# Kernel tuning notes

Hardware: AMD Instinct MI355X
Metric: run time of the kernel (lower is better)

Reference implementation:

```python
import jax, jax.numpy as jnp
import numpy as np

D_MODEL = 192
D_STATE = 16
D_CONV = 3
EXPAND = 2
D_INNER = EXPAND * D_MODEL  # 384
DT_RANK = (D_MODEL + 15) // 16  # 12 ('auto' = ceil(d_model/16))
B, H, W = 4, 48, 48


def setup_inputs() -> dict:
    key = jax.random.key(0)
    ks = jax.random.split(key, 8)
    s = 0.02
    n = lambda k, sh: (jax.random.normal(k, sh) * s).astype(jnp.float32)
    # 4 Mamba param sets stacked: [w_fwd, w_rev, h_fwd, h_rev]
    return {
        "x": jax.random.normal(ks[0], (B, H, W, D_MODEL), jnp.float32),
        "in_proj_w": n(ks[1], (4, 2 * D_INNER, D_MODEL)),
        "conv_w": n(ks[2], (4, D_INNER, D_CONV)),
        "conv_b": n(ks[3], (4, D_INNER)),
        "x_proj_w": n(ks[4], (4, DT_RANK + 2 * D_STATE, D_INNER)),
        "dt_proj_w": (jax.random.normal(ks[5], (4, D_INNER, DT_RANK)) * (DT_RANK ** -0.5)).astype(jnp.float32),
        "dt_proj_b": (-4.6 + 0.5 * jax.random.normal(ks[6], (4, D_INNER))).astype(jnp.float32),
        "A_log": jnp.broadcast_to(jnp.log(jnp.arange(1, D_STATE + 1, dtype=jnp.float32)), (4, D_INNER, D_STATE)) + jnp.zeros((4, D_INNER, D_STATE), jnp.float32),
        "D": jnp.ones((4, D_INNER), jnp.float32),
        "out_proj_w": n(ks[7], (4, D_MODEL, D_INNER)),
        "norm_w": jnp.ones((D_MODEL,), jnp.float32),
        "norm_b": jnp.zeros((D_MODEL,), jnp.float32),
    }


def _causal_conv(x, w, b):
    # x: [B,L,Di], w: [Di,K] depthwise, causal (pad left K-1, truncate to L)
    K = w.shape[1]
    L = x.shape[1]
    xp = jnp.pad(x, ((0, 0), (K - 1, 0), (0, 0)))
    y = b
    for k in range(K):
        y = y + xp[:, k:k + L, :] * w[:, k]
    return y


def _mamba(u, inW, cW, cB, xpW, dtW, dtB, Alog, Dp, outW):
    # u: [B,L,C]
    R = dtW.shape[1]
    N = Alog.shape[1]
    xz = u @ inW.T                         # [B,L,2*Di]
    xh, z = jnp.split(xz, 2, axis=-1)
    xc = jax.nn.silu(_causal_conv(xh, cW, cB))  # [B,L,Di]
    xdbl = xc @ xpW.T                      # [B,L,R+2N]
    dt = xdbl[..., :R]
    Bm = xdbl[..., R:R + N]
    Cm = xdbl[..., R + N:]
    delta = jax.nn.softplus(dt @ dtW.T + dtB)   # [B,L,Di]
    A = -jnp.exp(Alog)                     # [Di,N]

    def step(h, t):
        d_t, u_t, b_t, c_t = t             # [B,Di],[B,Di],[B,N],[B,N]
        h = jnp.exp(d_t[..., None] * A) * h + (d_t * u_t)[..., None] * b_t[:, None, :]
        return h, jnp.sum(h * c_t[:, None, :], axis=-1)

    h0 = jnp.zeros((u.shape[0], Alog.shape[0], N), u.dtype)
    _, ys = jax.lax.scan(step, h0, (jnp.swapaxes(delta, 0, 1), jnp.swapaxes(xc, 0, 1), jnp.swapaxes(Bm, 0, 1), jnp.swapaxes(Cm, 0, 1)))
    y = jnp.swapaxes(ys, 0, 1) + xc * Dp   # [B,L,Di]
    return (y * jax.nn.silu(z)) @ outW.T   # [B,L,C]


def _bimamba(u, i, P):
    p = lambda j: tuple(t[j] for t in P)
    # NOTE: per the original code, reversed-branch output is NOT flipped back
    return _mamba(u, *p(i)) + _mamba(u[:, ::-1], *p(i + 1))


def _ln(x, w, b):
    m = x.mean(-1, keepdims=True)
    v = ((x - m) ** 2).mean(-1, keepdims=True)
    return (x - m) / jnp.sqrt(v + 1e-5) * w + b


def reference(x, in_proj_w, conv_w, conv_b, x_proj_w, dt_proj_w, dt_proj_b, A_log, D, out_proj_w, norm_w, norm_b):
    Bb, Hh, Ww, C = x.shape
    P = (in_proj_w, conv_w, conv_b, x_proj_w, dt_proj_w, dt_proj_b, A_log, D, out_proj_w)
    # 'b h w c -> b (w h) c'
    xw = jnp.swapaxes(x, 1, 2).reshape(Bb, Ww * Hh, C)
    xw = _bimamba(xw, 0, P)
    # 'b (w h) c -> b (h w) c'
    xh = jnp.swapaxes(xw.reshape(Bb, Ww, Hh, C), 1, 2).reshape(Bb, Hh * Ww, C)
    xh = _ln(xh, norm_w, norm_b) + x.reshape(Bb, -1, C)
    xh = _bimamba(xh, 2, P)
    return xh.reshape(Bb, Hh, Ww, C)
```

## Files before the change

kernel.cpp:

```cpp
#include <hip/hip_runtime.h>
#include <math.h>

#define NB 4
#define NH 48
#define NW 48
#define NC 192
#define NL 2304
#define NM 9216
#define DIN 384
#define XD 44
#define DTR 12
#define CH 24
#define NCHUNK 96

typedef __attribute__((ext_vector_type(8))) short bf16x8;
typedef __attribute__((ext_vector_type(4))) float f32x4;

__device__ inline short f2bf(float f) {
  unsigned u = __builtin_bit_cast(unsigned, f);
  unsigned r = (u + 0x7fffu + ((u >> 16) & 1u)) >> 16;
  return (short)r;
}
__device__ inline float bf2f(short s) {
  unsigned u = ((unsigned)(unsigned short)s) << 16;
  return __builtin_bit_cast(float, u);
}
__device__ inline float fexp2(float x) { return __builtin_amdgcn_exp2f(x); }
__device__ inline float flog2(float x) { return __builtin_amdgcn_logf(x); }
#define LOG2E 1.4426950408889634f
#define LN2   0.6931471805599453f

#define GBM 128
#define GBN 64
#define GBK 32
__global__ __launch_bounds__(256) void mgemm(
    const float* __restrict__ A, int lda,
    const float* __restrict__ Wt,
    float* __restrict__ Cm, int ldc,
    int N, int K, int zA, int zW, int zC)
{
  A  += (size_t)blockIdx.z * zA;
  Wt += (size_t)blockIdx.z * zW;
  Cm += (size_t)blockIdx.z * zC;
  __shared__ short AsH[4][GBM+2][8], AsL[4][GBM+2][8];
  __shared__ short BsH[4][GBN+2][8], BsL[4][GBN+2][8];
  const int tid = threadIdx.x;
  const int l = tid & 63;
  const int wv = tid >> 6;
  const int wr = wv >> 1, wc = wv & 1;
  const int bm = blockIdx.y * GBM;
  const int bn = blockIdx.x * GBN;
  const int lrow = l & 15;
  const int lkb = l >> 4;

  f32x4 acc[4][2];
  #pragma unroll
  for (int mi = 0; mi < 4; ++mi)
    #pragma unroll
    for (int ni = 0; ni < 2; ++ni) acc[mi][ni] = (f32x4)0.f;

  for (int k0 = 0; k0 < K; k0 += GBK) {
    #pragma unroll
    for (int i = 0; i < 2; ++i) {
      int o = tid + i*256;
      int row = o >> 2, kb = o & 3;
      const float* src = A + (size_t)(bm + row)*lda + k0 + kb*8;
      float4 v0 = *(const float4*)src;
      float4 v1 = *(const float4*)(src + 4);
      float vv[8] = {v0.x,v0.y,v0.z,v0.w,v1.x,v1.y,v1.z,v1.w};
      bf16x8 hi, lo;
      #pragma unroll
      for (int j = 0; j < 8; ++j) {
        short h = f2bf(vv[j]);
        hi[j] = h;
        lo[j] = f2bf(vv[j] - bf2f(h));
      }
      *(bf16x8*)&AsH[kb][row][0] = hi;
      *(bf16x8*)&AsL[kb][row][0] = lo;
    }
    {
      int n = tid >> 2, kb = tid & 3;
      float4 v0 = make_float4(0.f,0.f,0.f,0.f), v1 = v0;
      if (bn + n < N) {
        const float* src = Wt + (size_t)(bn + n)*K + k0 + kb*8;
        v0 = *(const float4*)src;
        v1 = *(const float4*)(src + 4);
      }
      float vv[8] = {v0.x,v0.y,v0.z,v0.w,v1.x,v1.y,v1.z,v1.w};
      bf16x8 hi, lo;
      #pragma unroll
      for (int j = 0; j < 8; ++j) {
        short h = f2bf(vv[j]);
        hi[j] = h;
        lo[j] = f2bf(vv[j] - bf2f(h));
      }
      *(bf16x8*)&BsH[kb][n][0] = hi;
      *(bf16x8*)&BsL[kb][n][0] = lo;
    }
    __syncthreads();
    bf16x8 ah[4], al[4], bh[2], bl[2];
    #pragma unroll
    for (int mi = 0; mi < 4; ++mi) {
      int row = wr*64 + mi*16 + lrow;
      ah[mi] = *(const bf16x8*)&AsH[lkb][row][0];
      al[mi] = *(const bf16x8*)&AsL[lkb][row][0];
    }
    #pragma unroll
    for (int ni = 0; ni < 2; ++ni) {
      int rn = wc*32 + ni*16 + lrow;
      bh[ni] = *(const bf16x8*)&BsH[lkb][rn][0];
      bl[ni] = *(const bf16x8*)&BsL[lkb][rn][0];
    }
    #pragma unroll
    for (int mi = 0; mi < 4; ++mi)
      #pragma unroll
      for (int ni = 0; ni < 2; ++ni) {
        acc[mi][ni] = __builtin_amdgcn_mfma_f32_16x16x32_bf16(ah[mi], bh[ni], acc[mi][ni], 0, 0, 0);
        acc[mi][ni] = __builtin_amdgcn_mfma_f32_16x16x32_bf16(ah[mi], bl[ni], acc[mi][ni], 0, 0, 0);
        acc[mi][ni] = __builtin_amdgcn_mfma_f32_16x16x32_bf16(al[mi], bh[ni], acc[mi][ni], 0, 0, 0);
      }
    __syncthreads();
  }
  #pragma unroll
  for (int mi = 0; mi < 4; ++mi)
    #pragma unroll
    for (int ni = 0; ni < 2; ++ni) {
      int n = bn + wc*32 + ni*16 + lrow;
      if (n < N) {
        #pragma unroll
        for (int r = 0; r < 4; ++r) {
          int m = bm + wr*64 + mi*16 + lkb*4 + r;
          Cm[(size_t)m*ldc + n] = acc[mi][ni][r];
        }
      }
    }
}

__global__ __launch_bounds__(256) void transpose_in(const float* __restrict__ x, float* __restrict__ u1)
{
  int idx = blockIdx.x*256 + threadIdx.x;
  int c = idx % NC;
  int rr = idx / NC;
  int s1 = rr % NL;
  int b  = rr / NL;
  int hh = s1 % NH;
  int ww = s1 / NH;
  u1[idx] = x[(((size_t)b*NH + hh)*NW + ww)*NC + c];
}

__global__ __launch_bounds__(256) void conv_silu(
    const float* __restrict__ xz, const float* __restrict__ cw, const float* __restrict__ cb,
    float* __restrict__ xc, int pi)
{
  int idx = blockIdx.x*256 + threadIdx.x;
  int d2 = idx % 768;
  int r  = idx / 768;
  int s  = r % NL;
  int dir = d2 / 384;
  int d = d2 - dir*384;
  int p = pi + dir;
  const float* w = cw + ((size_t)p*DIN + d)*3;
  float acc = cb[p*DIN + d];
  const float* col = xz + (size_t)(r - s)*1536 + (dir*768 + d);
  if (dir == 0) {
    if (s >= 2) acc = fmaf(w[0], col[(size_t)(s-2)*1536], acc);
    if (s >= 1) acc = fmaf(w[1], col[(size_t)(s-1)*1536], acc);
    acc = fmaf(w[2], col[(size_t)s*1536], acc);
  } else {
    if (s+2 < NL) acc = fmaf(w[0], col[(size_t)(s+2)*1536], acc);
    if (s+1 < NL) acc = fmaf(w[1], col[(size_t)(s+1)*1536], acc);
    acc = fmaf(w[2], col[(size_t)s*1536], acc);
  }
  float sg = 1.f / (1.f + fexp2(-acc*LOG2E));
  xc[idx] = acc * sg;
}

__global__ __launch_bounds__(384) void scan_pass1(
    const float* __restrict__ xc, const float* __restrict__ xdbl,
    const float* __restrict__ dtw, const float* __restrict__ dtb,
    const float* __restrict__ alog, float* __restrict__ ws2,
    float* __restrict__ dlt_out, int pi)
{
  const int chunk = blockIdx.x;
  const int bd = blockIdx.y;
  const int b = bd >> 1, dir = bd & 1;
  const int d = threadIdx.x;
  const int p = pi + dir;
  __shared__ float sX[CH][28];
  for (int e = d; e < CH*28; e += 384) {
    int t = e / 28, q = e - t*28;
    int sseq = chunk*CH + t;
    int s = dir ? (NL-1-sseq) : sseq;
    sX[t][q] = xdbl[((size_t)b*NL + s)*88 + dir*XD + q];
  }
  float wdt[DTR];
  #pragma unroll
  for (int k = 0; k < DTR; ++k) wdt[k] = dtw[((size_t)p*DIN + d)*DTR + k];
  const float bdt = dtb[(size_t)p*DIN + d];
  float Ar2[16], h[16];
  #pragma unroll
  for (int n = 0; n < 16; ++n) {
    Ar2[n] = -__expf(alog[((size_t)p*DIN + d)*16 + n]) * LOG2E;
    h[n] = 0.f;
  }
  float cum = 0.f;
  __syncthreads();
  #pragma unroll 2
  for (int t = 0; t < CH; ++t) {
    int sseq = chunk*CH + t;
    int s = dir ? (NL-1-sseq) : sseq;
    size_t row = (size_t)b*NL + s;
    float u = xc[row*768 + dir*384 + d];
    float acc = bdt;
    #pragma unroll
    for (int k = 0; k < DTR; ++k) acc = fmaf(sX[t][k], wdt[k], acc);
    float e1 = fexp2(-fabsf(acc)*LOG2E);
    float dlt = fmaxf(acc, 0.f) + LN2*flog2(1.f + e1);
    cum += dlt;
    dlt_out[row*768 + dir*384 + d] = dlt;
    float du = dlt * u;
    #pragma unroll
    for (int n = 0; n < 16; ++n) {
      float a = fexp2(dlt * Ar2[n]);
      h[n] = fmaf(a, h[n], du * sX[t][12+n]);
    }
  }
  size_t base = ((size_t)bd*NCHUNK + chunk)*32*384 + d;
  #pragma unroll
  for (int n = 0; n < 16; ++n) {
    ws2[base + (size_t)n*384] = fexp2(cum * Ar2[n]);
    ws2[base + (size_t)(16+n)*384] = h[n];
  }
}

__global__ __launch_bounds__(256) void scan_prefix(float* __restrict__ ws2)
{
  int g = blockIdx.x*256 + threadIdx.x;
  int d = g % 384;
  int rest = g / 384;
  int n = rest & 15;
  int bd = rest >> 4;
  float hin = 0.f;
  size_t base = ((size_t)bd*NCHUNK*32 + n)*384 + d;
  for (int j = 0; j < NCHUNK; j += 8) {
    float Pv[8], hv[8];
    #pragma unroll
    for (int u = 0; u < 8; ++u) {
      size_t ip = base + (size_t)(j+u)*32*384;
      Pv[u] = ws2[ip];
      hv[u] = ws2[ip + (size_t)16*384];
    }
    #pragma unroll
    for (int u = 0; u < 8; ++u) {
      size_t ip = base + (size_t)(j+u)*32*384;
      ws2[ip + (size_t)16*384] = hin;
      hin = fmaf(Pv[u], hin, hv[u]);
    }
  }
}

__global__ __launch_bounds__(384) void scan_pass2(
    const float* __restrict__ xc, const float* __restrict__ xz,
    const float* __restrict__ xdbl, const float* __restrict__ alog,
    const float* __restrict__ dvec, const float* __restrict__ ws2,
    float* __restrict__ gio, int pi)
{
  const int chunk = blockIdx.x;
  const int bd = blockIdx.y;
  const int b = bd >> 1, dir = bd & 1;
  const int d = threadIdx.x;
  const int p = pi + dir;
  __shared__ float sX[CH][32];
  for (int e = d; e < CH*32; e += 384) {
    int t = e / 32, q = e - t*32;
    int sseq = chunk*CH + t;
    int s = dir ? (NL-1-sseq) : sseq;
    sX[t][q] = xdbl[((size_t)b*NL + s)*88 + dir*XD + 12 + q];
  }
  const float Dreg = dvec[(size_t)p*DIN + d];
  float Ar2[16], h[16];
  size_t base = ((size_t)bd*NCHUNK + chunk)*32*384 + d;
  #pragma unroll
  for (int n = 0; n < 16; ++n) {
    Ar2[n] = -__expf(alog[((size_t)p*DIN + d)*16 + n]) * LOG2E;
    h[n] = ws2[base + (size_t)(16+n)*384];
  }
  __syncthreads();
  #pragma unroll 2
  for (int t = 0; t < CH; ++t) {
    int sseq = chunk*CH + t;
    int s = dir ? (NL-1-sseq) : sseq;
    size_t row = (size_t)b*NL + s;
    size_t gidx = row*768 + dir*384 + d;
    float dlt = gio[gidx];
    float u = xc[gidx];
    float zv = xz[row*1536 + dir*768 + 384 + d];
    float du = dlt * u;
    float y = 0.f;
    #pragma unroll
    for (int n = 0; n < 16; ++n) {
      float a = fexp2(dlt * Ar2[n]);
      h[n] = fmaf(a, h[n], du * sX[t][n]);
      y = fmaf(h[n], sX[t][16+n], y);
    }
    y = fmaf(u, Dreg, y);
    float sg = 1.f / (1.f + fexp2(-zv*LOG2E));
    gio[gidx] = y * (zv * sg);
  }
}

__device__ inline float wave_sum(float v) {
  #pragma unroll
  for (int m = 1; m < 64; m <<= 1) v += __shfl_xor(v, m);
  return v;
}
__global__ __launch_bounds__(192) void ln_res(
    const float* __restrict__ ob0, const float* __restrict__ ob1,
    const float* __restrict__ x, const float* __restrict__ nw, const float* __restrict__ nb2,
    float* __restrict__ u2)
{
  int pb = blockIdx.x;
  int c = threadIdx.x;
  int b = pb / NL;
  int hw = pb % NL;
  int hh = hw / NW;
  int ww = hw % NW;
  int s1 = ww*NH + hh;
  float v = ob0[((size_t)b*NL + s1)*NC + c] + ob1[((size_t)b*NL + (NL-1-s1))*NC + c];
  __shared__ float red[6];
  float sv = wave_sum(v);
  int wid = c >> 6;
  if ((c & 63) == 0) red[wid] = sv;
  __syncthreads();
  float mean = (red[0]+red[1]+red[2]) * (1.f/NC);
  float dv = v - mean;
  float s2 = wave_sum(dv*dv);
  if ((c & 63) == 0) red[3+wid] = s2;
  __syncthreads();
  float var = (red[3]+red[4]+red[5]) * (1.f/NC);
  u2[(size_t)pb*NC + c] = dv * rsqrtf(var + 1e-5f) * nw[c] + nb2[c] + x[(size_t)pb*NC + c];
}

__global__ __launch_bounds__(256) void add_flip(
    const float* __restrict__ ob0, const float* __restrict__ ob1, float* __restrict__ out)
{
  int idx = blockIdx.x*256 + threadIdx.x;
  int c = idx % NC;
  int rr = idx / NC;
  int t = rr % NL;
  int b = rr / NL;
  out[idx] = ob0[idx] + ob1[((size_t)b*NL + (NL-1-t))*NC + c];
}

extern "C" void kernel_launch(void* const* d_in, const int* in_sizes, int n_in,
                              void* d_out, int out_size, void* d_ws, size_t ws_size,
                              hipStream_t stream)
{
  const float* x    = (const float*)d_in[0];
  const float* inw  = (const float*)d_in[1];
  const float* cw   = (const float*)d_in[2];
  const float* cb   = (const float*)d_in[3];
  const float* xpw  = (const float*)d_in[4];
  const float* dtw  = (const float*)d_in[5];
  const float* dtb  = (const float*)d_in[6];
  const float* alog = (const float*)d_in[7];
  const float* dvec = (const float*)d_in[8];
  const float* outw = (const float*)d_in[9];
  const float* nw   = (const float*)d_in[10];
  const float* nb   = (const float*)d_in[11];
  float* outp = (float*)d_out;
  (void)in_sizes; (void)n_in; (void)out_size; (void)ws_size;

  float* ws = (float*)d_ws;
  const size_t BLC = (size_t)NB*NL*NC;
  float* u1    = ws;
  float* xz    = u1 + BLC;
  float* xc    = xz + (size_t)NB*NL*1536;
  float* xdbl  = xc + (size_t)NB*NL*768;
  float* gbuf  = xdbl + (size_t)NB*NL*88;
  float* ws2   = gbuf + (size_t)NB*NL*768;
  float* ob0 = xc;
  float* ob1 = xc + BLC;

  transpose_in<<<(int)(BLC/256), 256, 0, stream>>>(x, u1);

  for (int layer = 0; layer < 2; ++layer) {
    int pi = layer*2;
    mgemm<<<dim3(1536/GBN, NM/GBM, 1), 256, 0, stream>>>(
        u1, NC, inw + (size_t)pi*768*NC, xz, 1536, 1536, NC, 0, 0, 0);
    conv_silu<<<NB*NL*768/256, 256, 0, stream>>>(xz, cw, cb, xc, pi);
    mgemm<<<dim3(1, NM/GBM, 2), 256, 0, stream>>>(
        xc, 768, xpw + (size_t)pi*XD*DIN, xdbl, 88, XD, DIN, 384, XD*DIN, XD);
    scan_pass1<<<dim3(NCHUNK, NB*2), 384, 0, stream>>>(xc, xdbl, dtw, dtb, alog, ws2, gbuf, pi);
    scan_prefix<<<192, 256, 0, stream>>>(ws2);
    scan_pass2<<<dim3(NCHUNK, NB*2), 384, 0, stream>>>(xc, xz, xdbl, alog, dvec, ws2, gbuf, pi);
    mgemm<<<dim3(NC/GBN, NM/GBM, 2), 256, 0, stream>>>(
        gbuf, 768, outw + (size_t)pi*NC*DIN, ob0, NC, NC, DIN, 384, NC*DIN, (int)BLC);
    if (layer == 0) {
      ln_res<<<NB*NL, NC, 0, stream>>>(ob0, ob1, x, nw, nb, u1);
    } else {
      add_flip<<<(int)(BLC/256), 256, 0, stream>>>(ob0, ob1, outp);
    }
  }
}
```

Baseline: 372.2 us.

## Halve scan chunk length and vectorize conv and scan shared-memory loads

The scan chunk length drops from 24 to 12 steps, doubling the number of chunks and blocks in scan_pass1 and scan_pass2. This raises parallelism on the sequential recurrence but doubles the chunk-state workspace traffic and the serial prefix length. conv_silu now handles four channels per thread with float4 loads and stores. The scan passes read dt weights and B/C coefficients as float4 vectors and load shared memory with one element per thread instead of a strided loop.

```diff
diff --git a/kernel.cpp b/kernel.cpp
--- a/kernel.cpp
+++ b/kernel.cpp
@@ -10,8 +10,8 @@
 #define DIN 384
 #define XD 44
 #define DTR 12
-#define CH 24
-#define NCHUNK 96
+#define CH 12
+#define NCHUNK 192
 
 typedef __attribute__((ext_vector_type(8))) short bf16x8;
 typedef __attribute__((ext_vector_type(4))) float f32x4;
@@ -153,26 +153,42 @@
     float* __restrict__ xc, int pi)
 {
   int idx = blockIdx.x*256 + threadIdx.x;
-  int d2 = idx % 768;
-  int r  = idx / 768;
-  int s  = r % NL;
+  int q = idx % 192;
+  int r = idx / 192;
+  int s = r % NL;
+  int d2 = q*4;
   int dir = d2 / 384;
   int d = d2 - dir*384;
   int p = pi + dir;
-  const float* w = cw + ((size_t)p*DIN + d)*3;
-  float acc = cb[p*DIN + d];
+  const float* wb = cw + ((size_t)p*DIN + d)*3;
+  float4 wa = *(const float4*)wb;
+  float4 wbv = *(const float4*)(wb+4);
+  float4 wcv = *(const float4*)(wb+8);
+  float4 w0 = make_float4(wa.x, wa.w, wbv.z, wcv.y);
+  float4 w1 = make_float4(wa.y, wbv.x, wbv.w, wcv.z);
+  float4 w2 = make_float4(wa.z, wbv.y, wcv.x, wcv.w);
+  float4 acc = *(const float4*)(cb + (size_t)p*DIN + d);
   const float* col = xz + (size_t)(r - s)*1536 + (dir*768 + d);
+  float4 t0, t1, t2;
   if (dir == 0) {
-    if (s >= 2) acc = fmaf(w[0], col[(size_t)(s-2)*1536], acc);
-    if (s >= 1) acc = fmaf(w[1], col[(size_t)(s-1)*1536], acc);
-    acc = fmaf(w[2], col[(size_t)s*1536], acc);
+    t2 = *(const float4*)(col + (size_t)s*1536);
+    t1 = (s >= 1) ? *(const float4*)(col + (size_t)(s-1)*1536) : make_float4(0,0,0,0);
+    t0 = (s >= 2) ? *(const float4*)(col + (size_t)(s-2)*1536) : make_float4(0,0,0,0);
   } else {
-    if (s+2 < NL) acc = fmaf(w[0], col[(size_t)(s+2)*1536], acc);
-    if (s+1 < NL) acc = fmaf(w[1], col[(size_t)(s+1)*1536], acc);
-    acc = fmaf(w[2], col[(size_t)s*1536], acc);
-  }
-  float sg = 1.f / (1.f + fexp2(-acc*LOG2E));
-  xc[idx] = acc * sg;
+    t2 = *(const float4*)(col + (size_t)s*1536);
+    t1 = (s+1 < NL) ? *(const float4*)(col + (size_t)(s+1)*1536) : make_float4(0,0,0,0);
+    t0 = (s+2 < NL) ? *(const float4*)(col + (size_t)(s+2)*1536) : make_float4(0,0,0,0);
+  }
+  float4 o;
+  o.x = fmaf(w0.x, t0.x, fmaf(w1.x, t1.x, fmaf(w2.x, t2.x, acc.x)));
+  o.y = fmaf(w0.y, t0.y, fmaf(w1.y, t1.y, fmaf(w2.y, t2.y, acc.y)));
+  o.z = fmaf(w0.z, t0.z, fmaf(w1.z, t1.z, fmaf(w2.z, t2.z, acc.z)));
+  o.w = fmaf(w0.w, t0.w, fmaf(w1.w, t1.w, fmaf(w2.w, t2.w, acc.w)));
+  o.x *= 1.f / (1.f + fexp2(-o.x*LOG2E));
+  o.y *= 1.f / (1.f + fexp2(-o.y*LOG2E));
+  o.z *= 1.f / (1.f + fexp2(-o.z*LOG2E));
+  o.w *= 1.f / (1.f + fexp2(-o.w*LOG2E));
+  *(float4*)(xc + (size_t)r*768 + d2) = o;
 }
 
 __global__ __launch_bounds__(384) void scan_pass1(
@@ -187,15 +203,15 @@
   const int d = threadIdx.x;
   const int p = pi + dir;
   __shared__ float sX[CH][28];
-  for (int e = d; e < CH*28; e += 384) {
-    int t = e / 28, q = e - t*28;
+  if (d < CH*28) {
+    int t = d / 28, q = d - t*28;
     int sseq = chunk*CH + t;
     int s = dir ? (NL-1-sseq) : sseq;
     sX[t][q] = xdbl[((size_t)b*NL + s)*88 + dir*XD + q];
   }
-  float wdt[DTR];
-  #pragma unroll
-  for (int k = 0; k < DTR; ++k) wdt[k] = dtw[((size_t)p*DIN + d)*DTR + k];
+  float4 wdt0 = *(const float4*)(dtw + ((size_t)p*DIN + d)*DTR);
+  float4 wdt1 = *(const float4*)(dtw + ((size_t)p*DIN + d)*DTR + 4);
+  float4 wdt2 = *(const float4*)(dtw + ((size_t)p*DIN + d)*DTR + 8);
   const float bdt = dtb[(size_t)p*DIN + d];
   float Ar2[16], h[16];
   #pragma unroll
@@ -211,18 +227,29 @@
     int s = dir ? (NL-1-sseq) : sseq;
     size_t row = (size_t)b*NL + s;
     float u = xc[row*768 + dir*384 + d];
+    float4 x0 = *(const float4*)&sX[t][0];
+    float4 x1 = *(const float4*)&sX[t][4];
+    float4 x2 = *(const float4*)&sX[t][8];
     float acc = bdt;
-    #pragma unroll
-    for (int k = 0; k < DTR; ++k) acc = fmaf(sX[t][k], wdt[k], acc);
+    acc = fmaf(x0.x, wdt0.x, acc); acc = fmaf(x0.y, wdt0.y, acc);
+    acc = fmaf(x0.z, wdt0.z, acc); acc = fmaf(x0.w, wdt0.w, acc);
+    acc = fmaf(x1.x, wdt1.x, acc); acc = fmaf(x1.y, wdt1.y, acc);
+    acc = fmaf(x1.z, wdt1.z, acc); acc = fmaf(x1.w, wdt1.w, acc);
+    acc = fmaf(x2.x, wdt2.x, acc); acc = fmaf(x2.y, wdt2.y, acc);
+    acc = fmaf(x2.z, wdt2.z, acc); acc = fmaf(x2.w, wdt2.w, acc);
     float e1 = fexp2(-fabsf(acc)*LOG2E);
     float dlt = fmaxf(acc, 0.f) + LN2*flog2(1.f + e1);
     cum += dlt;
     dlt_out[row*768 + dir*384 + d] = dlt;
     float du = dlt * u;
+    float4 B4[4];
+    #pragma unroll
+    for (int i = 0; i < 4; ++i) B4[i] = *(const float4*)&sX[t][12 + 4*i];
     #pragma unroll
     for (int n = 0; n < 16; ++n) {
       float a = fexp2(dlt * Ar2[n]);
-      h[n] = fmaf(a, h[n], du * sX[t][12+n]);
+      float bn = (n&3)==0 ? B4[n>>2].x : (n&3)==1 ? B4[n>>2].y : (n&3)==2 ? B4[n>>2].z : B4[n>>2].w;
+      h[n] = fmaf(a, h[n], du * bn);
     }
   }
   size_t base = ((size_t)bd*NCHUNK + chunk)*32*384 + d;
@@ -271,8 +298,8 @@
   const int d = threadIdx.x;
   const int p = pi + dir;
   __shared__ float sX[CH][32];
-  for (int e = d; e < CH*32; e += 384) {
-    int t = e / 32, q = e - t*32;
+  {
+    int t = d >> 5, q = d & 31;
     int sseq = chunk*CH + t;
     int s = dir ? (NL-1-sseq) : sseq;
     sX[t][q] = xdbl[((size_t)b*NL + s)*88 + dir*XD + 12 + q];
@@ -296,12 +323,20 @@
     float u = xc[gidx];
     float zv = xz[row*1536 + dir*768 + 384 + d];
     float du = dlt * u;
+    float4 B4[4], C4[4];
+    #pragma unroll
+    for (int i = 0; i < 4; ++i) {
+      B4[i] = *(const float4*)&sX[t][4*i];
+      C4[i] = *(const float4*)&sX[t][16 + 4*i];
+    }
     float y = 0.f;
     #pragma unroll
     for (int n = 0; n < 16; ++n) {
       float a = fexp2(dlt * Ar2[n]);
-      h[n] = fmaf(a, h[n], du * sX[t][n]);
-      y = fmaf(h[n], sX[t][16+n], y);
+      float bn = (n&3)==0 ? B4[n>>2].x : (n&3)==1 ? B4[n>>2].y : (n&3)==2 ? B4[n>>2].z : B4[n>>2].w;
+      float cn = (n&3)==0 ? C4[n>>2].x : (n&3)==1 ? C4[n>>2].y : (n&3)==2 ? C4[n>>2].z : C4[n>>2].w;
+      h[n] = fmaf(a, h[n], du * bn);
+      y = fmaf(h[n], cn, y);
     }
     y = fmaf(u, Dreg, y);
     float sg = 1.f / (1.f + fexp2(-zv*LOG2E));
@@ -388,7 +423,7 @@
     int pi = layer*2;
     mgemm<<<dim3(1536/GBN, NM/GBM, 1), 256, 0, stream>>>(
         u1, NC, inw + (size_t)pi*768*NC, xz, 1536, 1536, NC, 0, 0, 0);
-    conv_silu<<<NB*NL*768/256, 256, 0, stream>>>(xz, cw, cb, xc, pi);
+    conv_silu<<<NB*NL*192/256, 256, 0, stream>>>(xz, cw, cb, xc, pi);
     mgemm<<<dim3(1, NM/GBM, 2), 256, 0, stream>>>(
         xc, 768, xpw + (size_t)pi*XD*DIN, xdbl, 88, XD, DIN, 384, XD*DIN, XD);
     scan_pass1<<<dim3(NCHUNK, NB*2), 384, 0, stream>>>(xc, xdbl, dtw, dtb, alog, ws2, gbuf, pi);
```

Result: slower. 393.5 us (+5.7%).
